# Kernel tuning notes

Measured on AMD Instinct MI355X. Metric: run time of the kernel, lower is better.

The kernel has to match this reference:

```python
import jax, jax.numpy as jnp
import numpy as np

B, N, F = 4, 4096, 6
N_CENTROIDS, NSAMPLES, RADIUS = 1024, 64, 0.2


def fps(coords, n_c):
    # iterative farthest point sampling, vectorized over batch
    Bb, Nn, _ = coords.shape
    batch = jnp.arange(Bb)
    first = jnp.zeros((Bb,), jnp.int32)
    init_dist = jnp.full((Bb, Nn), 1e9, coords.dtype)

    def step(carry, _):
        dist, last = carry
        p = coords[batch, last]                      # (B,3) last chosen point
        d = jnp.sum((coords - p[:, None, :]) ** 2, -1)
        dist = jnp.minimum(dist, d)
        nxt = jnp.argmax(dist, -1).astype(jnp.int32)
        return (dist, nxt), nxt

    _, rest = jax.lax.scan(step, (init_dist, first), None, length=n_c - 1)
    return jnp.concatenate([first[None, :], rest], 0).T  # (B, n_c)


def ball_query(coords, centroids, radius, s):
    # coords (B,N,3), centroids (B,C,3) -> (B,C,S) neighbor indices
    Nn = coords.shape[1]
    d = jnp.sum((centroids[:, :, None, :] - coords[:, None, :, :]) ** 2, -1)  # (B,C,N)
    idx = jnp.where(d > radius * radius, Nn, jnp.arange(Nn))
    idx = jnp.sort(idx, axis=-1)[..., :s]
    first = idx[..., :1]                              # centroid itself always valid
    return jnp.where(idx == Nn, first, idx)


def tnet(h, w1, w2, w3, f1, f2):
    # h: (B, P, ch) -> (B, ch, ch) transform matrix (T-Net)
    ch = h.shape[-1]
    t = jax.nn.relu(h @ w1)
    t = jax.nn.relu(t @ w2)
    t = jax.nn.relu(t @ w3)
    t = t.max(axis=1)                                 # global max pool over points
    t = jax.nn.relu(t @ f1)
    return (t @ f2).reshape(-1, ch, ch) + jnp.eye(ch, dtype=h.dtype)


def setup_inputs() -> dict:
    key = jax.random.key(0)
    ks = jax.random.split(key, 20)
    sc = 0.02
    p = lambda k, shape: sc * jax.random.normal(k, shape, dtype=jnp.float32)
    return {
        'x': jax.random.normal(ks[0], (B, N, F), dtype=jnp.float32),
        'points': jax.random.uniform(ks[1], (B, N, 3), dtype=jnp.float32),
        # input T-Net (F x F)
        't1_w1': p(ks[2], (F, 64)), 't1_w2': p(ks[3], (64, 128)), 't1_w3': p(ks[4], (128, 256)),
        't1_f1': p(ks[5], (256, 128)), 't1_f2': p(ks[6], (128, F * F)),
        't2_w1': p(ks[7], (64, 64)), 't2_w2': p(ks[8], (64, 128)), 't2_w3': p(ks[9], (128, 256)),
        't2_f1': p(ks[10], (256, 128)), 't2_f2': p(ks[11], (128, 64 * 64)),
        # shared MLP
        'w1': p(ks[12], (F, 64)), 'w2': p(ks[13], (64, 128)), 'w3': p(ks[14], (128, 256)),
    }


def reference(x, points, t1_w1, t1_w2, t1_w3, t1_f1, t1_f2,
              t2_w1, t2_w2, t2_w3, t2_f1, t2_f2, w1, w2, w3):
    idx = fps(points, N_CENTROIDS)                                       # (B,C)
    centroids = jnp.take_along_axis(points, idx[..., None], axis=1)      # (B,C,3)
    gidx = ball_query(points, centroids, RADIUS, NSAMPLES)               # (B,C,S)
    gather = jax.vmap(lambda a, i: a[i])
    g_xyz = gather(points, gidx) - centroids[:, :, None, :]              # (B,C,S,3)
    g_feat = gather(x, gidx)                                             # (B,C,S,F)

    flat = g_feat.reshape(g_feat.shape[0], -1, g_feat.shape[-1])         # (B,C*S,F)
    inT = tnet(flat, t1_w1, t1_w2, t1_w3, t1_f1, t1_f2)                  # (B,F,F)
    h = jnp.einsum('bpc,bcd->bpd', flat, inT)
    h = jax.nn.relu(h @ w1)                                              # (B,C*S,64)
    feT = tnet(h, t2_w1, t2_w2, t2_w3, t2_f1, t2_f2)                     # (B,64,64)
    h = jnp.einsum('bpc,bcd->bpd', h, feT)
    h = jax.nn.relu(h @ w2)
    h = jax.nn.relu(h @ w3)                                              # (B,C*S,256)
    feats = h.reshape(h.shape[0], N_CENTROIDS, NSAMPLES, -1).max(axis=2) # (B,C,256)
    feats = feats.transpose(0, 2, 1)                                     # (B,256,C)
    return centroids, g_xyz.transpose(0, 3, 1, 2), feats, inT, feT
```

## Files before the change

kernel.cpp:

```cpp
#include <hip/hip_runtime.h>

#define Bb 4
#define Np 4096
#define Ff 6
#define NC 1024
#define NSAMP 64
#define NPTS (Bb*Np)
#define R2 ((float)(0.2*0.2))

static __host__ __device__ constexpr size_t alup(size_t x){ return (x + 255) & ~(size_t)255; }
static constexpr size_t OFF_GIDX = 0;
static constexpr size_t SZ_GIDX  = (size_t)Bb*NC*NSAMP*4;
static constexpr size_t OFF_MASK = alup(OFF_GIDX + SZ_GIDX);
static constexpr size_t SZ_MASK  = (size_t)Bb*Np*4;
static constexpr size_t OFF_T1   = OFF_MASK + SZ_MASK;
static constexpr size_t OFF_T2   = OFF_T1 + (size_t)Bb*256*4;
static constexpr size_t ZERO_BYTES = (OFF_T2 + (size_t)Bb*256*4) - OFF_MASK;
static constexpr size_t OFF_INT  = alup(OFF_T2 + (size_t)Bb*256*4);
static constexpr size_t OFF_FET  = alup(OFF_INT + (size_t)Bb*36*4);
static constexpr size_t OFF_XT    = alup(OFF_FET + (size_t)Bb*4096*4);
static constexpr size_t OFF_HW    = alup(OFF_XT + (size_t)6*NPTS*4);
static constexpr size_t OFF_BUF64 = alup(OFF_HW + (size_t)64*NPTS*4);
static constexpr size_t OFF_BUF128= alup(OFF_BUF64 + (size_t)64*NPTS*4);
static constexpr size_t OFF_FINAL = alup(OFF_BUF128 + (size_t)128*NPTS*4);

__device__ __forceinline__ unsigned wave_red_umax(unsigned v)
{
#define DPP_STEP(ctrl) { unsigned t = (unsigned)__builtin_amdgcn_update_dpp((int)v, (int)v, ctrl, 0xF, 0xF, false); v = (t > v) ? t : v; }
    DPP_STEP(0x111)
    DPP_STEP(0x112)
    DPP_STEP(0x114)
    DPP_STEP(0x118)
    DPP_STEP(0x142)
    DPP_STEP(0x143)
#undef DPP_STEP
    return v;
}

__global__ __launch_bounds__(512) void fps_kernel(const float* __restrict__ points,
                                                  float* __restrict__ out_cent)
{
    int b = blockIdx.x;
    const float* P = points + (size_t)b * Np * 3;
    int tid  = threadIdx.x;
    int lane = tid & 63;
    int wave = tid >> 6;

    __shared__ float4 sc[Np];
    __shared__ __align__(16) uint2 swin[2][8];

    float px[8], py[8], pz[8], dist[8];
#pragma unroll
    for (int j = 0; j < 8; ++j) {
        int p = tid + 512 * j;
        float x = P[p*3+0], y = P[p*3+1], z = P[p*3+2];
        px[j] = x; py[j] = y; pz[j] = z;
        dist[j] = 1000000000.0f;
        sc[p] = make_float4(x, y, z, 0.f);
    }
    __syncthreads();

    float cx = sc[0].x, cy = sc[0].y, cz = sc[0].z;
    if (tid == 0) {
        out_cent[((size_t)b*NC + 0)*3 + 0] = cx;
        out_cent[((size_t)b*NC + 0)*3 + 1] = cy;
        out_cent[((size_t)b*NC + 0)*3 + 2] = cz;
    }

    for (int s = 1; s < NC; ++s) {
        float m = -1.0f;
#pragma unroll
        for (int j = 0; j < 8; ++j) {
            float dx = __fsub_rn(px[j], cx);
            float dy = __fsub_rn(py[j], cy);
            float dz = __fsub_rn(pz[j], cz);
            float d  = __fadd_rn(__fadd_rn(__fmul_rn(dx,dx), __fmul_rn(dy,dy)), __fmul_rn(dz,dz));
            float nd = fminf(dist[j], d);
            dist[j] = nd;
            m = fmaxf(m, nd);
        }
        unsigned pi = 0u;
#pragma unroll
        for (int j = 7; j >= 0; --j)
            pi = (dist[j] == m) ? (unsigned)(tid + (j << 9)) : pi;

        unsigned mb = __float_as_uint(m);
        unsigned mr = wave_red_umax(mb);
        unsigned maxd = (unsigned)__builtin_amdgcn_readlane((int)mr, 63);
        unsigned cand = (mb == maxd) ? ~pi : 0u;
        unsigned cr = wave_red_umax(cand);
        if (lane == 63) swin[s & 1][wave] = make_uint2(mr, cr);
        __syncthreads();

        const uint4* sw = (const uint4*)&swin[s & 1][0];
        uint4 q0 = sw[0], q1 = sw[1], q2 = sw[2], q3 = sw[3];
        double k0 = fmax(__hiloint2double((int)q0.x, (int)q0.y), __hiloint2double((int)q0.z, (int)q0.w));
        double k1 = fmax(__hiloint2double((int)q1.x, (int)q1.y), __hiloint2double((int)q1.z, (int)q1.w));
        double k2 = fmax(__hiloint2double((int)q2.x, (int)q2.y), __hiloint2double((int)q2.z, (int)q2.w));
        double k3 = fmax(__hiloint2double((int)q3.x, (int)q3.y), __hiloint2double((int)q3.z, (int)q3.w));
        double kk = fmax(fmax(k0, k1), fmax(k2, k3));
        int widx = (int)(~(unsigned)__double2loint(kk));

        float4 c = sc[widx];
        cx = c.x; cy = c.y; cz = c.z;
        if (tid == 0) {
            out_cent[((size_t)b*NC + s)*3 + 0] = cx;
            out_cent[((size_t)b*NC + s)*3 + 1] = cy;
            out_cent[((size_t)b*NC + s)*3 + 2] = cz;
        }
    }
}

__global__ __launch_bounds__(256) void ballq_kernel(const float* __restrict__ points,
                                                    const float* __restrict__ cent,
                                                    int* __restrict__ gidx,
                                                    int* __restrict__ mask,
                                                    float* __restrict__ out_gxyz)
{
    int gtid = blockIdx.x * 256 + threadIdx.x;
    int wid  = gtid >> 6;
    int lane = threadIdx.x & 63;
    int b = wid >> 10, c = wid & 1023;
    const float* P = points + (size_t)b * Np * 3;
    float cx = cent[((size_t)b*NC + c)*3 + 0];
    float cy = cent[((size_t)b*NC + c)*3 + 1];
    float cz = cent[((size_t)b*NC + c)*3 + 2];

    __shared__ int sidx[4][NSAMP];
    int* my = sidx[threadIdx.x >> 6];

    int count = 0;
    for (int base = 0; base < Np; base += 64) {
        int p = base + lane;
        float dx = __fsub_rn(cx, P[p*3+0]);
        float dy = __fsub_rn(cy, P[p*3+1]);
        float dz = __fsub_rn(cz, P[p*3+2]);
        float d  = __fadd_rn(__fadd_rn(__fmul_rn(dx,dx), __fmul_rn(dy,dy)), __fmul_rn(dz,dz));
        bool inr = !(d > R2);
        unsigned long long mball = __ballot(inr);
        int before = __popcll(mball & ((1ull << lane) - 1ull));
        int pos = count + before;
        if (inr && pos < NSAMP) my[pos] = p;
        count += (int)__popcll(mball);
        if (count >= NSAMP) break;
    }
    __syncthreads();
    int total = count < NSAMP ? count : NSAMP;
    int first = my[0];
    int myi = (lane < total) ? my[lane] : first;
    gidx[(size_t)wid * NSAMP + lane] = myi;
    mask[(size_t)b * Np + myi] = 1;
    float qx = P[myi*3+0], qy = P[myi*3+1], qz = P[myi*3+2];
    out_gxyz[(((size_t)b*3 + 0)*NC + c)*NSAMP + lane] = __fsub_rn(qx, cx);
    out_gxyz[(((size_t)b*3 + 1)*NC + c)*NSAMP + lane] = __fsub_rn(qy, cy);
    out_gxyz[(((size_t)b*3 + 2)*NC + c)*NSAMP + lane] = __fsub_rn(qz, cz);
}

__global__ __launch_bounds__(256) void xpose_kernel(const float* __restrict__ x, float* __restrict__ xT)
{
    int id = blockIdx.x * 256 + threadIdx.x;
    if (id < Ff * NPTS) {
        int ch = id >> 14;
        int g  = id & (NPTS-1);
        xT[id] = x[(size_t)g * Ff + ch];
    }
}

template<int K, int N, int NT, bool RELU, bool PM, bool BW, bool TM>
__global__ __launch_bounds__(256) void layer2_k(const float* __restrict__ in,
                                                const float* __restrict__ W,
                                                float* __restrict__ out,
                                                const int* __restrict__ mask,
                                                unsigned* __restrict__ tmax)
{
    int tid = threadIdx.x;
    int g0  = blockIdx.x * 1024 + tid;
    int o0  = blockIdx.y * NT;
    const float* Wb = W;
    if (BW) Wb += (size_t)(blockIdx.x >> 2) * K * N;

    __shared__ float ws[K * NT];
    for (int i = tid; i < K * NT; i += 256)
        ws[i] = Wb[(size_t)(i / NT) * N + o0 + (i % NT)];
    __syncthreads();

    float acc[4][NT];
#pragma unroll
    for (int mi = 0; mi < 4; ++mi)
#pragma unroll
        for (int oo = 0; oo < NT; ++oo) acc[mi][oo] = 0.f;

#pragma unroll 4
    for (int k = 0; k < K; ++k) {
        float a0 = in[(size_t)k * NPTS + g0];
        float a1 = in[(size_t)k * NPTS + g0 + 256];
        float a2 = in[(size_t)k * NPTS + g0 + 512];
        float a3 = in[(size_t)k * NPTS + g0 + 768];
#pragma unroll
        for (int oo = 0; oo < NT; ++oo) {
            float w = ws[k * NT + oo];
            acc[0][oo] += a0 * w;
            acc[1][oo] += a1 * w;
            acc[2][oo] += a2 * w;
            acc[3][oo] += a3 * w;
        }
    }

    if (TM) {
        float tmv[NT];
#pragma unroll
        for (int oo = 0; oo < NT; ++oo) tmv[oo] = 0.f;
#pragma unroll
        for (int mi = 0; mi < 4; ++mi) {
            bool pres = mask[g0 + mi * 256] != 0;
#pragma unroll
            for (int oo = 0; oo < NT; ++oo) {
                float v = pres ? fmaxf(acc[mi][oo], 0.f) : 0.f;
                tmv[oo] = fmaxf(tmv[oo], v);
            }
        }
        int b = g0 >> 12;
        int lane = tid & 63;
#pragma unroll
        for (int oo = 0; oo < NT; ++oo) {
            unsigned r = wave_red_umax(__float_as_uint(tmv[oo]));
            if (lane == 63)
                atomicMax(&tmax[(b << 8) + o0 + oo], r);
        }
        return;
    }

#pragma unroll
    for (int mi = 0; mi < 4; ++mi) {
        int g = g0 + mi * 256;
#pragma unroll
        for (int oo = 0; oo < NT; ++oo) {
            float v = acc[mi][oo];
            if (RELU) v = fmaxf(v, 0.f);
            if (PM) out[(size_t)g * N + o0 + oo] = v;
            else    out[(size_t)(o0 + oo) * NPTS + g] = v;
        }
    }
}

__global__ __launch_bounds__(256) void l_h_kernel(const float* __restrict__ xT,
                                                  const float* __restrict__ inT,
                                                  const float* __restrict__ w1,
                                                  float* __restrict__ hw)
{
    int g = blockIdx.x * 256 + threadIdx.x;
    int b = g >> 12;
    float v[6];
#pragma unroll
    for (int c = 0; c < 6; ++c) v[c] = xT[(size_t)c * NPTS + g];
    float t[6];
#pragma unroll
    for (int o = 0; o < 6; ++o) {
        float acc = 0.f;
#pragma unroll
        for (int c = 0; c < 6; ++c) acc += v[c] * inT[b*36 + c*6 + o];
        t[o] = acc;
    }
#pragma unroll 8
    for (int j = 0; j < 64; ++j) {
        float acc = 0.f;
#pragma unroll
        for (int o = 0; o < 6; ++o) acc += t[o] * w1[o*64 + j];
        hw[(size_t)j * NPTS + g] = fmaxf(acc, 0.f);
    }
}

__global__ __launch_bounds__(256) void head1_kernel(const float* __restrict__ t1,
                                                    const float* __restrict__ f1,
                                                    const float* __restrict__ f2,
                                                    float* __restrict__ outT, float* __restrict__ wsT)
{
    int b = blockIdx.x, t = threadIdx.x;
    __shared__ float tv[256], u[128];
    tv[t] = t1[(size_t)b*256 + t];
    __syncthreads();
    if (t < 128) {
        float acc = 0.f;
        for (int k = 0; k < 256; ++k) acc += tv[k] * f1[(size_t)k*128 + t];
        u[t] = fmaxf(acc, 0.f);
    }
    __syncthreads();
    if (t < 36) {
        float acc = 0.f;
        for (int k = 0; k < 128; ++k) acc += u[k] * f2[(size_t)k*36 + t];
        if (t / 6 == t % 6) acc += 1.0f;
        outT[b*36 + t] = acc;
        wsT[b*36 + t]  = acc;
    }
}

__global__ __launch_bounds__(256) void head2_kernel(const float* __restrict__ t2,
                                                    const float* __restrict__ f1,
                                                    const float* __restrict__ f2,
                                                    float* __restrict__ outT, float* __restrict__ wsT)
{
    int b = blockIdx.x, t = threadIdx.x;
    __shared__ float tv[256], u[128];
    tv[t] = t2[(size_t)b*256 + t];
    __syncthreads();
    if (t < 128) {
        float acc = 0.f;
        for (int k = 0; k < 256; ++k) acc += tv[k] * f1[(size_t)k*128 + t];
        u[t] = fmaxf(acc, 0.f);
    }
    __syncthreads();
    int j = blockIdx.y * 256 + t;
    float acc = 0.f;
#pragma unroll 8
    for (int k = 0; k < 128; ++k) acc += u[k] * f2[(size_t)k*4096 + j];
    if (j / 64 == j % 64) acc += 1.0f;
    outT[(size_t)b*4096 + j] = acc;
    wsT[(size_t)b*4096 + j]  = acc;
}

__global__ __launch_bounds__(256) void feats_kernel(const float* __restrict__ fin,
                                                    const int* __restrict__ gidx,
                                                    float* __restrict__ out)
{
    int bid = blockIdx.x;
    int b = bid >> 10, c = bid & 1023;
    int o = threadIdx.x;
    __shared__ int sid[NSAMP];
    if (o < NSAMP) sid[o] = gidx[(size_t)bid * NSAMP + o];
    __syncthreads();
    const float* fb = fin + (size_t)b * Np * 256;
    float m = -1e30f;
    for (int s = 0; s < NSAMP; ++s)
        m = fmaxf(m, fb[(size_t)sid[s] * 256 + o]);
    out[((size_t)b*256 + o)*NC + c] = m;
}

extern "C" void kernel_launch(void* const* d_in, const int* in_sizes, int n_in,
                              void* d_out, int out_size, void* d_ws, size_t ws_size,
                              hipStream_t stream)
{
    const float* x      = (const float*)d_in[0];
    const float* points = (const float*)d_in[1];
    const float* t1_w1  = (const float*)d_in[2];
    const float* t1_w2  = (const float*)d_in[3];
    const float* t1_w3  = (const float*)d_in[4];
    const float* t1_f1  = (const float*)d_in[5];
    const float* t1_f2  = (const float*)d_in[6];
    const float* t2_w1  = (const float*)d_in[7];
    const float* t2_w2  = (const float*)d_in[8];
    const float* t2_w3  = (const float*)d_in[9];
    const float* t2_f1  = (const float*)d_in[10];
    const float* t2_f2  = (const float*)d_in[11];
    const float* w1     = (const float*)d_in[12];
    const float* w2     = (const float*)d_in[13];
    const float* w3     = (const float*)d_in[14];

    float* out = (float*)d_out;
    float* out_cent  = out;
    float* out_gxyz  = out + 12288;
    float* out_feats = out + 798720;
    float* out_inT   = out + 1847296;
    float* out_feT   = out + 1847440;

    char* ws = (char*)d_ws;
    int*      gidx  = (int*)(ws + OFF_GIDX);
    int*      mask  = (int*)(ws + OFF_MASK);
    unsigned* t1max = (unsigned*)(ws + OFF_T1);
    unsigned* t2max = (unsigned*)(ws + OFF_T2);
    float*    wsInT = (float*)(ws + OFF_INT);
    float*    wsFeT = (float*)(ws + OFF_FET);
    float*    xT    = (float*)(ws + OFF_XT);
    float*    hw    = (float*)(ws + OFF_HW);
    float*    buf64 = (float*)(ws + OFF_BUF64);
    float*    buf128= (float*)(ws + OFF_BUF128);
    float*    fin   = (float*)(ws + OFF_FINAL);

    hipMemsetAsync(ws + OFF_MASK, 0, ZERO_BYTES, stream);

    fps_kernel<<<Bb, 512, 0, stream>>>(points, out_cent);
    ballq_kernel<<<(Bb*NC)/4, 256, 0, stream>>>(points, out_cent, gidx, mask, out_gxyz);
    xpose_kernel<<<(Ff*NPTS + 255)/256, 256, 0, stream>>>(x, xT);

    layer2_k<6,  64, 16, true,  false, false, false><<<dim3(16, 4), 256, 0, stream>>>(xT,    t1_w1, buf64,  nullptr, nullptr);
    layer2_k<64, 128,16, true,  false, false, false><<<dim3(16, 8), 256, 0, stream>>>(buf64, t1_w2, buf128, nullptr, nullptr);
    layer2_k<128,256,16, false, false, false, true ><<<dim3(16,16), 256, 0, stream>>>(buf128,t1_w3, nullptr, mask, t1max);
    head1_kernel<<<Bb, 256, 0, stream>>>((const float*)t1max, t1_f1, t1_f2, out_inT, wsInT);
    l_h_kernel<<<NPTS/256, 256, 0, stream>>>(xT, wsInT, w1, hw);
    layer2_k<64, 64, 16, true,  false, false, false><<<dim3(16, 4), 256, 0, stream>>>(hw,    t2_w1, buf64,  nullptr, nullptr);
    layer2_k<64, 128,16, true,  false, false, false><<<dim3(16, 8), 256, 0, stream>>>(buf64, t2_w2, buf128, nullptr, nullptr);
    layer2_k<128,256,16, false, false, false, true ><<<dim3(16,16), 256, 0, stream>>>(buf128,t2_w3, nullptr, mask, t2max);
    head2_kernel<<<dim3(Bb,16), 256, 0, stream>>>((const float*)t2max, t2_f1, t2_f2, out_feT, wsFeT);
    layer2_k<64, 64, 16, false, false, true,  false><<<dim3(16, 4), 256, 0, stream>>>(hw,    wsFeT, buf64,  nullptr, nullptr);
    layer2_k<64, 128,16, true,  false, false, false><<<dim3(16, 8), 256, 0, stream>>>(buf64, w2,    buf128, nullptr, nullptr);
    layer2_k<128,256,16, true,  true,  false, false><<<dim3(16,16), 256, 0, stream>>>(buf128,w3,    fin,    nullptr, nullptr);
    feats_kernel<<<Bb*NC, 256, 0, stream>>>(fin, gidx, out_feats);

    (void)in_sizes; (void)n_in; (void)out_size; (void)ws_size;
}
```

Before: 920.0 us.

## Streamline FPS argmax with packed f64 keys, fuse transpose, vectorize weight loads

The FPS kernel now uses 256 threads holding 16 points each and packs (distance, ~index) into a double key. One DPP max-reduction per wave then replaces the two-pass max-then-index reduction, and the cross-wave combine reads only 4 entries. The x transpose runs in extra blocks of the FPS launch, saving one kernel launch. The layer GEMM reads weights from shared memory as float4 with a smaller unroll. These changes target the serial per-iteration latency of the 1023-step FPS loop, at the cost of more registers per thread and f64 DPP operations.

```diff
diff --git a/kernel.cpp b/kernel.cpp
--- a/kernel.cpp
+++ b/kernel.cpp
@@ -37,9 +37,30 @@
     return v;
 }
 
-__global__ __launch_bounds__(512) void fps_kernel(const float* __restrict__ points,
-                                                  float* __restrict__ out_cent)
-{
+template<int CTRL>
+__device__ __forceinline__ double dpp_max_f64(double v)
+{
+    int lo = __double2loint(v), hi = __double2hiint(v);
+    int tlo = __builtin_amdgcn_update_dpp(lo, lo, CTRL, 0xF, 0xF, false);
+    int thi = __builtin_amdgcn_update_dpp(hi, hi, CTRL, 0xF, 0xF, false);
+    return fmax(v, __hiloint2double(thi, tlo));
+}
+
+__global__ __launch_bounds__(256) void fps_kernel(const float* __restrict__ points,
+                                                  float* __restrict__ out_cent,
+                                                  const float* __restrict__ x,
+                                                  float* __restrict__ xT)
+{
+    if (blockIdx.x >= Bb) {
+        int id = (blockIdx.x - Bb) * 256 + threadIdx.x;
+        if (id < Ff * NPTS) {
+            int ch = id >> 14;
+            int g  = id & (NPTS-1);
+            xT[id] = x[(size_t)g * Ff + ch];
+        }
+        return;
+    }
+
     int b = blockIdx.x;
     const float* P = points + (size_t)b * Np * 3;
     int tid  = threadIdx.x;
@@ -47,16 +68,18 @@
     int wave = tid >> 6;
 
     __shared__ float4 sc[Np];
-    __shared__ __align__(16) uint2 swin[2][8];
-
-    float px[8], py[8], pz[8], dist[8];
-#pragma unroll
-    for (int j = 0; j < 8; ++j) {
-        int p = tid + 512 * j;
-        float x = P[p*3+0], y = P[p*3+1], z = P[p*3+2];
-        px[j] = x; py[j] = y; pz[j] = z;
+    __shared__ __align__(16) double swin[2][4];
+
+    float px[16], py[16], pz[16], dist[16];
+    int ilo[16];
+#pragma unroll
+    for (int j = 0; j < 16; ++j) {
+        int p = tid + (j << 8);
+        float xx = P[p*3+0], yy = P[p*3+1], zz = P[p*3+2];
+        px[j] = xx; py[j] = yy; pz[j] = zz;
         dist[j] = 1000000000.0f;
-        sc[p] = make_float4(x, y, z, 0.f);
+        ilo[j] = ~p;
+        sc[p] = make_float4(xx, yy, zz, 0.f);
     }
     __syncthreads();
 
@@ -68,38 +91,35 @@
     }
 
     for (int s = 1; s < NC; ++s) {
-        float m = -1.0f;
-#pragma unroll
-        for (int j = 0; j < 8; ++j) {
+        double k0 = -1.0, k1 = -1.0, k2 = -1.0, k3 = -1.0;
+#pragma unroll
+        for (int j = 0; j < 16; ++j) {
             float dx = __fsub_rn(px[j], cx);
             float dy = __fsub_rn(py[j], cy);
             float dz = __fsub_rn(pz[j], cz);
             float d  = __fadd_rn(__fadd_rn(__fmul_rn(dx,dx), __fmul_rn(dy,dy)), __fmul_rn(dz,dz));
             float nd = fminf(dist[j], d);
             dist[j] = nd;
-            m = fmaxf(m, nd);
-        }
-        unsigned pi = 0u;
-#pragma unroll
-        for (int j = 7; j >= 0; --j)
-            pi = (dist[j] == m) ? (unsigned)(tid + (j << 9)) : pi;
-
-        unsigned mb = __float_as_uint(m);
-        unsigned mr = wave_red_umax(mb);
-        unsigned maxd = (unsigned)__builtin_amdgcn_readlane((int)mr, 63);
-        unsigned cand = (mb == maxd) ? ~pi : 0u;
-        unsigned cr = wave_red_umax(cand);
-        if (lane == 63) swin[s & 1][wave] = make_uint2(mr, cr);
+            double kj = __hiloint2double(__float_as_int(nd), ilo[j]);
+            if      ((j & 3) == 0) k0 = fmax(k0, kj);
+            else if ((j & 3) == 1) k1 = fmax(k1, kj);
+            else if ((j & 3) == 2) k2 = fmax(k2, kj);
+            else                   k3 = fmax(k3, kj);
+        }
+        double key = fmax(fmax(k0, k1), fmax(k2, k3));
+        key = dpp_max_f64<0x111>(key);
+        key = dpp_max_f64<0x112>(key);
+        key = dpp_max_f64<0x114>(key);
+        key = dpp_max_f64<0x118>(key);
+        key = dpp_max_f64<0x142>(key);
+        key = dpp_max_f64<0x143>(key);
+        if (lane == 63) swin[s & 1][wave] = key;
         __syncthreads();
 
-        const uint4* sw = (const uint4*)&swin[s & 1][0];
-        uint4 q0 = sw[0], q1 = sw[1], q2 = sw[2], q3 = sw[3];
-        double k0 = fmax(__hiloint2double((int)q0.x, (int)q0.y), __hiloint2double((int)q0.z, (int)q0.w));
-        double k1 = fmax(__hiloint2double((int)q1.x, (int)q1.y), __hiloint2double((int)q1.z, (int)q1.w));
-        double k2 = fmax(__hiloint2double((int)q2.x, (int)q2.y), __hiloint2double((int)q2.z, (int)q2.w));
-        double k3 = fmax(__hiloint2double((int)q3.x, (int)q3.y), __hiloint2double((int)q3.z, (int)q3.w));
-        double kk = fmax(fmax(k0, k1), fmax(k2, k3));
-        int widx = (int)(~(unsigned)__double2loint(kk));
+        const double2* sw = (const double2*)&swin[s & 1][0];
+        double2 p01 = sw[0], p23 = sw[1];
+        double kk = fmax(fmax(p01.x, p01.y), fmax(p23.x, p23.y));
+        int widx = ~__double2loint(kk);
 
         float4 c = sc[widx];
         cx = c.x; cy = c.y; cz = c.z;
@@ -156,16 +176,6 @@
     out_gxyz[(((size_t)b*3 + 2)*NC + c)*NSAMP + lane] = __fsub_rn(qz, cz);
 }
 
-__global__ __launch_bounds__(256) void xpose_kernel(const float* __restrict__ x, float* __restrict__ xT)
-{
-    int id = blockIdx.x * 256 + threadIdx.x;
-    if (id < Ff * NPTS) {
-        int ch = id >> 14;
-        int g  = id & (NPTS-1);
-        xT[id] = x[(size_t)g * Ff + ch];
-    }
-}
-
 template<int K, int N, int NT, bool RELU, bool PM, bool BW, bool TM>
 __global__ __launch_bounds__(256) void layer2_k(const float* __restrict__ in,
                                                 const float* __restrict__ W,
@@ -173,13 +183,14 @@
                                                 const int* __restrict__ mask,
                                                 unsigned* __restrict__ tmax)
 {
+    static_assert(NT % 4 == 0, "NT multiple of 4");
     int tid = threadIdx.x;
     int g0  = blockIdx.x * 1024 + tid;
     int o0  = blockIdx.y * NT;
     const float* Wb = W;
     if (BW) Wb += (size_t)(blockIdx.x >> 2) * K * N;
 
-    __shared__ float ws[K * NT];
+    __shared__ __align__(16) float ws[K * NT];
     for (int i = tid; i < K * NT; i += 256)
         ws[i] = Wb[(size_t)(i / NT) * N + o0 + (i % NT)];
     __syncthreads();
@@ -190,19 +201,24 @@
 #pragma unroll
         for (int oo = 0; oo < NT; ++oo) acc[mi][oo] = 0.f;
 
-#pragma unroll 4
+#pragma unroll 2
     for (int k = 0; k < K; ++k) {
         float a0 = in[(size_t)k * NPTS + g0];
         float a1 = in[(size_t)k * NPTS + g0 + 256];
         float a2 = in[(size_t)k * NPTS + g0 + 512];
         float a3 = in[(size_t)k * NPTS + g0 + 768];
-#pragma unroll
-        for (int oo = 0; oo < NT; ++oo) {
-            float w = ws[k * NT + oo];
-            acc[0][oo] += a0 * w;
-            acc[1][oo] += a1 * w;
-            acc[2][oo] += a2 * w;
-            acc[3][oo] += a3 * w;
+        const float4* wr = (const float4*)&ws[k * NT];
+#pragma unroll
+        for (int q = 0; q < NT/4; ++q) {
+            float4 w = wr[q];
+            acc[0][4*q+0] += a0 * w.x;  acc[0][4*q+1] += a0 * w.y;
+            acc[0][4*q+2] += a0 * w.z;  acc[0][4*q+3] += a0 * w.w;
+            acc[1][4*q+0] += a1 * w.x;  acc[1][4*q+1] += a1 * w.y;
+            acc[1][4*q+2] += a1 * w.z;  acc[1][4*q+3] += a1 * w.w;
+            acc[2][4*q+0] += a2 * w.x;  acc[2][4*q+1] += a2 * w.y;
+            acc[2][4*q+2] += a2 * w.z;  acc[2][4*q+3] += a2 * w.w;
+            acc[3][4*q+0] += a3 * w.x;  acc[3][4*q+1] += a3 * w.y;
+            acc[3][4*q+2] += a3 * w.z;  acc[3][4*q+3] += a3 * w.w;
         }
     }
 
@@ -375,11 +391,10 @@
     float*    buf128= (float*)(ws + OFF_BUF128);
     float*    fin   = (float*)(ws + OFF_FINAL);
 
-    hipMemsetAsync(ws + OFF_MASK, 0, ZERO_BYTES, stream);
-
-    fps_kernel<<<Bb, 512, 0, stream>>>(points, out_cent);
+    (void)hipMemsetAsync(ws + OFF_MASK, 0, ZERO_BYTES, stream);
+
+    fps_kernel<<<Bb + (Ff*NPTS + 255)/256, 256, 0, stream>>>(points, out_cent, x, xT);
     ballq_kernel<<<(Bb*NC)/4, 256, 0, stream>>>(points, out_cent, gidx, mask, out_gxyz);
-    xpose_kernel<<<(Ff*NPTS + 255)/256, 256, 0, stream>>>(x, xT);
 
     layer2_k<6,  64, 16, true,  false, false, false><<<dim3(16, 4), 256, 0, stream>>>(xT,    t1_w1, buf64,  nullptr, nullptr);
     layer2_k<64, 128,16, true,  false, false, false><<<dim3(16, 8), 256, 0, stream>>>(buf64, t1_w2, buf128, nullptr, nullptr);
```

Result: faster. 791.1 us (-14.0%).
